# Kernel optimization log

Hardware: AMD Instinct MI355X
Metric: run time of the kernel (lower is better)

The kernel has to match this reference:

```python
import jax, jax.numpy as jnp
import numpy as np

B, C, N, T = 64, 8, 2048, 64


def setup_inputs() -> dict:
    key = jax.random.key(0)
    k1, k2, k3 = jax.random.split(key, 3)
    x = jax.random.normal(k1, (B, C, N, T), dtype=jnp.float32)
    Wc = jax.random.normal(k2, (T, T), dtype=jnp.float32) * 0.05
    alpha = jax.random.normal(k3, (N,), dtype=jnp.float32) * 0.05
    return {"x": x, "Wc": Wc, "alpha": alpha}


def reference(x, Wc, alpha):
    # k = q = einsum('bcit,i->bct'): learned node-weighted reduction -> [B, C, T]
    k = jnp.einsum('bcit,i->bct', x, alpha)
    # bilinear channel scores: k @ Wc @ q^T -> [B, C, C]
    scores = jnp.einsum('bct,ts,bds->bcd', k, Wc, k)
    att = jax.nn.softmax(scores, axis=-1)
    # aggregate channels: einsum('bci,bint->bcnt') -> [B, C, N, T]
    return jnp.einsum('bci,bint->bcnt', att, x)
```

## Files before the change

kernel.cpp:

```cpp
#include <hip/hip_runtime.h>

#define BB 64
#define CC 8
#define NN 2048
#define TT 64

__global__ __launch_bounds__(256) void k_reduce(const float* __restrict__ x,
                                                const float* __restrict__ alpha,
                                                float* __restrict__ kout) {
    const int bc  = blockIdx.x;
    const int tid = threadIdx.x;
    const int t4  = tid & 15;
    const int ig  = tid >> 4;
    const float4* xp = (const float4*)(x + (size_t)bc * NN * TT);
    float4 acc = make_float4(0.f, 0.f, 0.f, 0.f);
    for (int i = ig; i < NN; i += 16) {
        const float  a = alpha[i];
        const float4 v = xp[i * 16 + t4];
        acc.x += a * v.x; acc.y += a * v.y; acc.z += a * v.z; acc.w += a * v.w;
    }
    __shared__ float4 part[16][16];
    part[ig][t4] = acc;
    __syncthreads();
    for (int s = 8; s > 0; s >>= 1) {
        if (ig < s) {
            const float4 o = part[ig + s][t4];
            acc.x += o.x; acc.y += o.y; acc.z += o.z; acc.w += o.w;
            part[ig][t4] = acc;
        }
        __syncthreads();
    }
    if (ig == 0) {
        ((float4*)(kout + (size_t)bc * TT))[t4] = acc;
    }
}

__global__ __launch_bounds__(64) void att_kernel(const float* __restrict__ kin,
                                                 const float* __restrict__ Wc,
                                                 float* __restrict__ att) {
    const int b = blockIdx.x;
    const int t = threadIdx.x;
    __shared__ float kS[CC][TT];
    __shared__ float mS[CC][TT];
    for (int d = 0; d < CC; ++d)
        kS[d][t] = kin[((size_t)b * CC + d) * TT + t];
    __syncthreads();
    float m[CC];
    for (int d = 0; d < CC; ++d) m[d] = 0.f;
    for (int s = 0; s < TT; ++s) {
        const float w = Wc[t * TT + s];
        for (int d = 0; d < CC; ++d) m[d] += w * kS[d][s];
    }
    for (int d = 0; d < CC; ++d) mS[d][t] = m[d];
    __syncthreads();
    const int c = t >> 3, d = t & 7;
    float sc = 0.f;
    for (int tt = 0; tt < TT; ++tt) sc += kS[c][tt] * mS[d][tt];
    float mx = sc;
    for (int off = 1; off < 8; off <<= 1)
        mx = fmaxf(mx, __shfl_xor(mx, off, 8));
    const float e = __expf(sc - mx);
    float sum = e;
    for (int off = 1; off < 8; off <<= 1)
        sum += __shfl_xor(sum, off, 8);
    att[(size_t)b * CC * CC + t] = e / sum;
}

__global__ __launch_bounds__(256) void agg_kernel(const float* __restrict__ x,
                                                  const float* __restrict__ att,
                                                  float* __restrict__ out) {
    const int b     = blockIdx.x >> 7;
    const int ntile = blockIdx.x & 127;
    const int tid   = threadIdx.x;
    __shared__ float attS[CC * CC];
    if (tid < CC * CC) attS[tid] = att[(size_t)b * CC * CC + tid];
    __syncthreads();
    const int n  = ntile * 16 + (tid >> 4);
    const int t4 = tid & 15;
    const size_t base = ((size_t)b * CC * NN + n) * TT + t4 * 4;
    float4 acc[CC];
    for (int c = 0; c < CC; ++c) acc[c] = make_float4(0.f, 0.f, 0.f, 0.f);
    for (int i = 0; i < CC; ++i) {
        const float4 v = *(const float4*)(x + base + (size_t)i * NN * TT);
        for (int c = 0; c < CC; ++c) {
            const float a = attS[c * CC + i];
            acc[c].x += a * v.x; acc[c].y += a * v.y;
            acc[c].z += a * v.z; acc[c].w += a * v.w;
        }
    }
    for (int c = 0; c < CC; ++c)
        *(float4*)(out + base + (size_t)c * NN * TT) = acc[c];
}

extern "C" void kernel_launch(void* const* d_in, const int* in_sizes, int n_in,
                              void* d_out, int out_size, void* d_ws, size_t ws_size,
                              hipStream_t stream) {
    const float* x     = (const float*)d_in[0];
    const float* Wc    = (const float*)d_in[1];
    const float* alpha = (const float*)d_in[2];
    float* out = (float*)d_out;

    float* kws   = (float*)d_ws;
    float* attws = kws + (size_t)BB * CC * TT;

    k_reduce<<<BB * CC, 256, 0, stream>>>(x, alpha, kws);
    att_kernel<<<BB, 64, 0, stream>>>(kws, Wc, attws);
    agg_kernel<<<BB * (NN / 16), 256, 0, stream>>>(x, attws, out);
}
```

Measured before the change: 490.2 us.

## Split node reduction across blocks, widen attention kernel, nontemporal output stores

The node-weighted reduction now splits N into four chunks per (b,c), giving four times as many blocks. Each block stages its alpha chunk in shared memory, and the partial sums are combined inside the attention kernel. The attention kernel grows to 256 threads, stages a transposed Wc in padded shared memory and spreads the Wc·k product across all threads. The aggregation kernel issues all eight input loads up front, fully unrolls the FMAs and writes the output with nontemporal stores to avoid polluting the cache; the cost is more workspace and an extra partial-sum pass.

```diff
diff --git a/kernel.cpp b/kernel.cpp
--- a/kernel.cpp
+++ b/kernel.cpp
@@ -4,21 +4,37 @@
 #define CC 8
 #define NN 2048
 #define TT 64
+#define NSPLIT 4
+#define NCHUNK (NN / NSPLIT)
 
-__global__ __launch_bounds__(256) void k_reduce(const float* __restrict__ x,
-                                                const float* __restrict__ alpha,
-                                                float* __restrict__ kout) {
-    const int bc  = blockIdx.x;
+typedef float f4_nt __attribute__((ext_vector_type(4)));
+
+__global__ __launch_bounds__(256) void k_partial(const float* __restrict__ x,
+                                                 const float* __restrict__ alpha,
+                                                 float* __restrict__ kp) {
+    const int bc  = blockIdx.x >> 2;
+    const int sp  = blockIdx.x & 3;
     const int tid = threadIdx.x;
     const int t4  = tid & 15;
     const int ig  = tid >> 4;
-    const float4* xp = (const float4*)(x + (size_t)bc * NN * TT);
+
+    __shared__ float aS[NCHUNK];
+    const int i0 = sp * NCHUNK;
+    for (int j = tid; j < NCHUNK; j += 256) aS[j] = alpha[i0 + j];
+    __syncthreads();
+
+    const float4* xp = (const float4*)(x + ((size_t)bc * NN + i0) * TT);
     float4 acc = make_float4(0.f, 0.f, 0.f, 0.f);
-    for (int i = ig; i < NN; i += 16) {
-        const float  a = alpha[i];
+    #pragma unroll 8
+    for (int i = ig; i < NCHUNK; i += 16) {
+        const float  a = aS[i];
         const float4 v = xp[i * 16 + t4];
-        acc.x += a * v.x; acc.y += a * v.y; acc.z += a * v.z; acc.w += a * v.w;
+        acc.x = fmaf(a, v.x, acc.x);
+        acc.y = fmaf(a, v.y, acc.y);
+        acc.z = fmaf(a, v.z, acc.z);
+        acc.w = fmaf(a, v.w, acc.w);
     }
+
     __shared__ float4 part[16][16];
     part[ig][t4] = acc;
     __syncthreads();
@@ -30,40 +46,64 @@
         }
         __syncthreads();
     }
-    if (ig == 0) {
-        ((float4*)(kout + (size_t)bc * TT))[t4] = acc;
-    }
+    if (ig == 0)
+        ((float4*)(kp + ((size_t)bc * NSPLIT + sp) * TT))[t4] = acc;
 }
 
-__global__ __launch_bounds__(64) void att_kernel(const float* __restrict__ kin,
-                                                 const float* __restrict__ Wc,
-                                                 float* __restrict__ att) {
-    const int b = blockIdx.x;
-    const int t = threadIdx.x;
-    __shared__ float kS[CC][TT];
-    __shared__ float mS[CC][TT];
-    for (int d = 0; d < CC; ++d)
-        kS[d][t] = kin[((size_t)b * CC + d) * TT + t];
+__global__ __launch_bounds__(256) void att_kernel(const float* __restrict__ kp,
+                                                  const float* __restrict__ Wc,
+                                                  float* __restrict__ att) {
+    const int b   = blockIdx.x;
+    const int tid = threadIdx.x;
+
+    __shared__ float wT[TT][TT + 1];
+    __shared__ float kS[CC][TT + 1];
+    __shared__ float mS[CC][TT + 1];
+
+    for (int idx = tid; idx < TT * TT / 4; idx += 256) {
+        const float4 w = ((const float4*)Wc)[idx];
+        const int t = idx >> 4;
+        const int s = (idx & 15) * 4;
+        wT[s + 0][t] = w.x;
+        wT[s + 1][t] = w.y;
+        wT[s + 2][t] = w.z;
+        wT[s + 3][t] = w.w;
+    }
+    for (int idx = tid; idx < CC * TT; idx += 256) {
+        const int c = idx >> 6, t = idx & 63;
+        float s = 0.f;
+        #pragma unroll
+        for (int sp = 0; sp < NSPLIT; ++sp)
+            s += kp[(((size_t)b * CC + c) * NSPLIT + sp) * TT + t];
+        kS[c][t] = s;
+    }
     __syncthreads();
-    float m[CC];
-    for (int d = 0; d < CC; ++d) m[d] = 0.f;
-    for (int s = 0; s < TT; ++s) {
-        const float w = Wc[t * TT + s];
-        for (int d = 0; d < CC; ++d) m[d] += w * kS[d][s];
+
+    for (int idx = tid; idx < CC * TT; idx += 256) {
+        const int d = idx >> 6, t = idx & 63;
+        float acc = 0.f;
+        #pragma unroll 8
+        for (int s = 0; s < TT; ++s)
+            acc = fmaf(wT[s][t], kS[d][s], acc);
+        mS[d][t] = acc;
     }
-    for (int d = 0; d < CC; ++d) mS[d][t] = m[d];
     __syncthreads();
-    const int c = t >> 3, d = t & 7;
-    float sc = 0.f;
-    for (int tt = 0; tt < TT; ++tt) sc += kS[c][tt] * mS[d][tt];
-    float mx = sc;
-    for (int off = 1; off < 8; off <<= 1)
-        mx = fmaxf(mx, __shfl_xor(mx, off, 8));
-    const float e = __expf(sc - mx);
-    float sum = e;
-    for (int off = 1; off < 8; off <<= 1)
-        sum += __shfl_xor(sum, off, 8);
-    att[(size_t)b * CC * CC + t] = e / sum;
+
+    if (tid < 64) {
+        const int c = tid >> 3, d = tid & 7;
+        float sc = 0.f;
+        #pragma unroll 8
+        for (int t = 0; t < TT; ++t)
+            sc = fmaf(kS[c][t], mS[d][t], sc);
+        float mx = sc;
+        for (int off = 1; off < 8; off <<= 1)
+            mx = fmaxf(mx, __shfl_xor(mx, off, 8));
+        const float e = __expf(sc - mx);
+        float sum = e;
+        for (int off = 1; off < 8; off <<= 1)
+            sum += __shfl_xor(sum, off, 8);
+        att[(size_t)b * CC * CC + tid] = e / sum;
+    }
 }
 
 __global__ __launch_bounds__(256) void agg_kernel(const float* __restrict__ x,
@@ -72,24 +112,39 @@
     const int b     = blockIdx.x >> 7;
     const int ntile = blockIdx.x & 127;
     const int tid   = threadIdx.x;
+
     __shared__ float attS[CC * CC];
     if (tid < CC * CC) attS[tid] = att[(size_t)b * CC * CC + tid];
     __syncthreads();
+
     const int n  = ntile * 16 + (tid >> 4);
     const int t4 = tid & 15;
     const size_t base = ((size_t)b * CC * NN + n) * TT + t4 * 4;
+
+    float4 v[CC];
+    #pragma unroll
+    for (int i = 0; i < CC; ++i)
+        v[i] = *(const float4*)(x + base + (size_t)i * NN * TT);
+
     float4 acc[CC];
+    #pragma unroll
     for (int c = 0; c < CC; ++c) acc[c] = make_float4(0.f, 0.f, 0.f, 0.f);
+    #pragma unroll
     for (int i = 0; i < CC; ++i) {
-        const float4 v = *(const float4*)(x + base + (size_t)i * NN * TT);
+        #pragma unroll
         for (int c = 0; c < CC; ++c) {
             const float a = attS[c * CC + i];
-            acc[c].x += a * v.x; acc[c].y += a * v.y;
-            acc[c].z += a * v.z; acc[c].w += a * v.w;
+            acc[c].x = fmaf(a, v[i].x, acc[c].x);
+            acc[c].y = fmaf(a, v[i].y, acc[c].y);
+            acc[c].z = fmaf(a, v[i].z, acc[c].z);
+            acc[c].w = fmaf(a, v[i].w, acc[c].w);
         }
     }
-    for (int c = 0; c < CC; ++c)
-        *(float4*)(out + base + (size_t)c * NN * TT) = acc[c];
+    #pragma unroll
+    for (int c = 0; c < CC; ++c) {
+        f4_nt val = { acc[c].x, acc[c].y, acc[c].z, acc[c].w };
+        __builtin_nontemporal_store(val, (f4_nt*)(out + base + (size_t)c * NN * TT));
+    }
 }
 
 extern "C" void kernel_launch(void* const* d_in, const int* in_sizes, int n_in,
@@ -100,10 +155,10 @@
     const float* alpha = (const float*)d_in[2];
     float* out = (float*)d_out;
 
-    float* kws   = (float*)d_ws;
-    float* attws = kws + (size_t)BB * CC * TT;
+    float* kpws  = (float*)d_ws;
+    float* attws = kpws + (size_t)BB * CC * NSPLIT * TT;
 
-    k_reduce<<<BB * CC, 256, 0, stream>>>(x, alpha, kws);
-    att_kernel<<<BB, 64, 0, stream>>>(kws, Wc, attws);
+    k_partial<<<BB * CC * NSPLIT, 256, 0, stream>>>(x, alpha, kpws);
+    att_kernel<<<BB, 256, 0, stream>>>(kpws, Wc, attws);
     agg_kernel<<<BB * (NN / 16), 256, 0, stream>>>(x, attws, out);
 }
```

Result: no change. 482.5 us (-1.6%).
